# Performance work log

Measured on AMD Instinct MI355X. Metric: run time of the kernel, lower is better.

## Reference

```python
import jax, jax.numpy as jnp
import numpy as np

IN_CH = 1024
OUT_CH = 1024
N_SUBJECTS = 32
B = 512


def setup_inputs() -> dict:
    key = jax.random.key(0)
    k_x, k_w, k_b, k_idx = jax.random.split(key, 4)
    scale = 1.0 / (IN_CH ** 0.5)
    x = jax.random.normal(k_x, (B, IN_CH), dtype=jnp.float32)
    weights = jax.random.normal(k_w, (N_SUBJECTS, IN_CH, OUT_CH), dtype=jnp.float32) * scale
    bias = jax.random.normal(k_b, (N_SUBJECTS, OUT_CH), dtype=jnp.float32) * scale
    subject_idx = jax.random.randint(k_idx, (B,), 0, N_SUBJECTS, dtype=jnp.int64)
    return {"x": x, "subject_idx": subject_idx, "weights": weights, "bias": bias}


def reference(x, subject_idx, weights, bias):
    # gather per-sample weight [B,C,D] and bias [B,D]
    w = weights[subject_idx]          # [B, C, D]
    b = bias[subject_idx]             # [B, D]
    out = jnp.einsum('bc,bcd->bd', x, w) + b
    return out
```

## Files before the change

kernel.cpp:

```cpp
#include <hip/hip_runtime.h>
#include <hip/hip_bf16.h>


typedef float f4v __attribute__((ext_vector_type(4)));

#define N_SUBJ 32
#define B_ROWS 512
#define IN_CH_K 1024
#define OUT_CH_K 1024
#define RPC 24
#define MAX_CHUNKS 64
#define CSEGS 4
#define CSEG 256
#define WSLICE 64
#define DTILES 4
#define DTILE 256
#define XPAD 28

#define ENT_OFF 1
#define PERM_OFF 256

__global__ __launch_bounds__(512) void build_groups(
    const int* __restrict__ idx, int* __restrict__ ws)
{
    __shared__ int counts[N_SUBJ];
    __shared__ int offs[N_SUBJ];
    __shared__ int cursor[N_SUBJ];
    const int t = threadIdx.x;
    if (t < N_SUBJ) counts[t] = 0;
    __syncthreads();
    const int s = idx[t] & (N_SUBJ - 1);
    atomicAdd(&counts[s], 1);
    __syncthreads();
    if (t == 0) {
        int acc = 0, nch = 0;
        for (int i = 0; i < N_SUBJ; ++i) {
            offs[i] = acc;
            cursor[i] = acc;
            acc += counts[i];
        }
        for (int i = 0; i < N_SUBJ; ++i) {
            for (int st = 0; st < counts[i]; st += RPC) {
                int c = counts[i] - st;
                if (c > RPC) c = RPC;
                ws[ENT_OFF + nch * 3 + 0] = i;
                ws[ENT_OFF + nch * 3 + 1] = offs[i] + st;
                ws[ENT_OFF + nch * 3 + 2] = c;
                ++nch;
            }
        }
        ws[0] = nch;
    }
    __syncthreads();
    const int pos = atomicAdd(&cursor[s], 1);
    ws[PERM_OFF + pos] = t;
}

__global__ __launch_bounds__(256) void init_bias(
    const int* __restrict__ idx, const float* __restrict__ bias,
    float* __restrict__ out)
{
    const int b = blockIdx.x;
    const int s = idx[b];
    const int d = threadIdx.x * 4;
    *(float4*)&out[(size_t)b * OUT_CH_K + d] =
        *(const float4*)&bias[(size_t)s * OUT_CH_K + d];
}

#define GLOAD(dst, ptr) \
    asm volatile("global_load_dwordx4 %0, %1, off" : "=v"(dst) : "v"(ptr))
#define WAIT_VM(n) do { \
    asm volatile("s_waitcnt vmcnt(" #n ")" ::: "memory"); \
    __builtin_amdgcn_sched_barrier(0); } while (0)

#define CSTEP(wreg, cidx) { \
    const float4 x0 = ((const float4*)&xst[cidx][0])[0]; \
    const float4 x1 = ((const float4*)&xst[cidx][0])[1]; \
    const float4 x2 = ((const float4*)&xst[cidx][0])[2]; \
    const float4 x3 = ((const float4*)&xst[cidx][0])[3]; \
    const float4 x4 = ((const float4*)&xst[cidx][0])[4]; \
    const float4 x5 = ((const float4*)&xst[cidx][0])[5]; \
    acc[ 0] += wreg * x0.x;  acc[ 1] += wreg * x0.y; \
    acc[ 2] += wreg * x0.z;  acc[ 3] += wreg * x0.w; \
    acc[ 4] += wreg * x1.x;  acc[ 5] += wreg * x1.y; \
    acc[ 6] += wreg * x1.z;  acc[ 7] += wreg * x1.w; \
    acc[ 8] += wreg * x2.x;  acc[ 9] += wreg * x2.y; \
    acc[10] += wreg * x2.z;  acc[11] += wreg * x2.w; \
    acc[12] += wreg * x3.x;  acc[13] += wreg * x3.y; \
    acc[14] += wreg * x3.z;  acc[15] += wreg * x3.w; \
    acc[16] += wreg * x4.x;  acc[17] += wreg * x4.y; \
    acc[18] += wreg * x4.z;  acc[19] += wreg * x4.w; \
    acc[20] += wreg * x5.x;  acc[21] += wreg * x5.y; \
    acc[22] += wreg * x5.z;  acc[23] += wreg * x5.w; }

__global__ __launch_bounds__(256, 2) void subject_gemm(
    const float* __restrict__ x, const float* __restrict__ W,
    const int* __restrict__ ws, float* __restrict__ out)
{
    const int chunk = blockIdx.x;
    if (chunk >= ws[0]) return;
    const int s     = ws[ENT_OFF + chunk * 3 + 0];
    const int start = ws[ENT_OFF + chunk * 3 + 1];
    const int cnt   = ws[ENT_OFF + chunk * 3 + 2];
    const int cbase = blockIdx.y * CSEG;
    const int dbase = blockIdx.z * DTILE;

    __shared__ float xst[CSEG][XPAD];
    __shared__ int rowidx[RPC];

    const int t = threadIdx.x;
    if (t < RPC)
        rowidx[t] = (t < cnt) ? ws[PERM_OFF + start + t] : -1;
    __syncthreads();

    #pragma unroll
    for (int r = 0; r < RPC; ++r) {
        const int row = rowidx[r];
        xst[t][r] = (row >= 0) ? x[(size_t)row * IN_CH_K + cbase + t] : 0.0f;
    }
    __syncthreads();

    const int lane = t & 63;
    const int wave = t >> 6;
    const int cs   = wave * WSLICE;
    const int d    = dbase + lane * 4;
    const float* wp = W + (size_t)s * (IN_CH_K * OUT_CH_K)
                        + (size_t)(cbase + cs) * OUT_CH_K + d;

    f4v acc[RPC];
    #pragma unroll
    for (int r = 0; r < RPC; ++r) acc[r] = (f4v){0.f, 0.f, 0.f, 0.f};
    f4v wa0, wa1, wa2, wa3, wb0, wb1, wb2, wb3;

    GLOAD(wa0, wp + 0 * OUT_CH_K);
    GLOAD(wa1, wp + 1 * OUT_CH_K);
    GLOAD(wa2, wp + 2 * OUT_CH_K);
    GLOAD(wa3, wp + 3 * OUT_CH_K);
    GLOAD(wb0, wp + 4 * OUT_CH_K);
    GLOAD(wb1, wp + 5 * OUT_CH_K);
    GLOAD(wb2, wp + 6 * OUT_CH_K);
    GLOAD(wb3, wp + 7 * OUT_CH_K);

    #pragma unroll 1
    for (int cb = 0; cb < WSLICE - 8; cb += 8) {
        WAIT_VM(4);
        CSTEP(wa0, cs + cb + 0)
        CSTEP(wa1, cs + cb + 1)
        CSTEP(wa2, cs + cb + 2)
        CSTEP(wa3, cs + cb + 3)
        const float* wn = wp + (size_t)(cb + 8) * OUT_CH_K;
        GLOAD(wa0, wn + 0 * OUT_CH_K);
        GLOAD(wa1, wn + 1 * OUT_CH_K);
        GLOAD(wa2, wn + 2 * OUT_CH_K);
        GLOAD(wa3, wn + 3 * OUT_CH_K);
        WAIT_VM(4);
        CSTEP(wb0, cs + cb + 4)
        CSTEP(wb1, cs + cb + 5)
        CSTEP(wb2, cs + cb + 6)
        CSTEP(wb3, cs + cb + 7)
        GLOAD(wb0, wn + 4 * OUT_CH_K);
        GLOAD(wb1, wn + 5 * OUT_CH_K);
        GLOAD(wb2, wn + 6 * OUT_CH_K);
        GLOAD(wb3, wn + 7 * OUT_CH_K);
    }
    {
        const int cb = WSLICE - 8;
        WAIT_VM(4);
        CSTEP(wa0, cs + cb + 0)
        CSTEP(wa1, cs + cb + 1)
        CSTEP(wa2, cs + cb + 2)
        CSTEP(wa3, cs + cb + 3)
        WAIT_VM(0);
        CSTEP(wb0, cs + cb + 4)
        CSTEP(wb1, cs + cb + 5)
        CSTEP(wb2, cs + cb + 6)
        CSTEP(wb3, cs + cb + 7)
    }

    __syncthreads();
    float (*obuf)[DTILE] = (float(*)[DTILE])&xst[0][0];
    if (wave == 0) {
        #pragma unroll
        for (int r = 0; r < RPC; ++r)
            *(f4v*)&obuf[r][lane * 4] = acc[r];
    }
    __syncthreads();
    #pragma unroll
    for (int w = 1; w < 4; ++w) {
        if (wave == w) {
            #pragma unroll
            for (int r = 0; r < RPC; ++r) {
                f4v v = *(const f4v*)&obuf[r][lane * 4];
                *(f4v*)&obuf[r][lane * 4] = v + acc[r];
            }
        }
        __syncthreads();
    }

    #pragma unroll
    for (int i = 0; i < 6; ++i) {
        const int r = wave * 6 + i;
        const int row = rowidx[r];
        if (row >= 0) {
            const f4v v = *(const f4v*)&obuf[r][lane * 4];
            float* o = &out[(size_t)row * OUT_CH_K + d];
            atomicAdd(o + 0, v.x); atomicAdd(o + 1, v.y);
            atomicAdd(o + 2, v.z); atomicAdd(o + 3, v.w);
        }
    }
}

extern "C" void kernel_launch(void* const* d_in, const int* in_sizes, int n_in,
                              void* d_out, int out_size, void* d_ws, size_t ws_size,
                              hipStream_t stream) {
    const float* x    = (const float*)d_in[0];
    const int*   idx  = (const int*)d_in[1];
    const float* W    = (const float*)d_in[2];
    const float* bias = (const float*)d_in[3];
    float* out = (float*)d_out;
    int* ws = (int*)d_ws;

    build_groups<<<1, 512, 0, stream>>>(idx, ws);
    init_bias<<<B_ROWS, 256, 0, stream>>>(idx, bias, out);

    dim3 grid(MAX_CHUNKS, CSEGS, DTILES);
    subject_gemm<<<grid, 256, 0, stream>>>(x, W, ws, out);
}
```

Before: 234.6 us.

## Split reduction into eight C segments with partial buffers and separate reduce kernel

Doubles the number of input-channel segments (CSEG 256→128), which doubles the GEMM grid so more blocks are available to cover the weight stream. Atomic float adds into the output are replaced by plain vector stores into per-segment partial buffers in workspace. A new reduce kernel sums the eight partials and adds the bias, and it replaces the old bias-init kernel. The cost is extra workspace traffic of 8×512×1024 floats written and read, plus the assumption that every (row, segment) partial slot is written, which holds because each row belongs to exactly one chunk.

New measurement: 233.3 us. Within noise of the previous version (-0.5%).

```diff
diff --git a/kernel.cpp b/kernel.cpp
--- a/kernel.cpp
+++ b/kernel.cpp
@@ -10,15 +10,16 @@
 #define OUT_CH_K 1024
 #define RPC 24
 #define MAX_CHUNKS 64
-#define CSEGS 4
-#define CSEG 256
-#define WSLICE 64
+#define CSEGS 8
+#define CSEG 128
+#define WSLICE 32
 #define DTILES 4
 #define DTILE 256
 #define XPAD 28
 
 #define ENT_OFF 1
 #define PERM_OFF 256
+#define PART_OFF_F 1024
 
 __global__ __launch_bounds__(512) void build_groups(
     const int* __restrict__ idx, int* __restrict__ ws)
@@ -54,17 +55,6 @@
     __syncthreads();
     const int pos = atomicAdd(&cursor[s], 1);
     ws[PERM_OFF + pos] = t;
-}
-
-__global__ __launch_bounds__(256) void init_bias(
-    const int* __restrict__ idx, const float* __restrict__ bias,
-    float* __restrict__ out)
-{
-    const int b = blockIdx.x;
-    const int s = idx[b];
-    const int d = threadIdx.x * 4;
-    *(float4*)&out[(size_t)b * OUT_CH_K + d] =
-        *(const float4*)&bias[(size_t)s * OUT_CH_K + d];
 }
 
 #define GLOAD(dst, ptr) \
@@ -95,7 +85,7 @@
 
 __global__ __launch_bounds__(256, 2) void subject_gemm(
     const float* __restrict__ x, const float* __restrict__ W,
-    const int* __restrict__ ws, float* __restrict__ out)
+    const int* __restrict__ ws, float* __restrict__ ws_part)
 {
     const int chunk = blockIdx.x;
     if (chunk >= ws[0]) return;
@@ -105,7 +95,8 @@
     const int cbase = blockIdx.y * CSEG;
     const int dbase = blockIdx.z * DTILE;
 
-    __shared__ float xst[CSEG][XPAD];
+    __shared__ float smem[RPC * DTILE];
+    float (*xst)[XPAD] = (float(*)[XPAD])smem;
     __shared__ int rowidx[RPC];
 
     const int t = threadIdx.x;
@@ -113,10 +104,13 @@
         rowidx[t] = (t < cnt) ? ws[PERM_OFF + start + t] : -1;
     __syncthreads();
 
-    #pragma unroll
-    for (int r = 0; r < RPC; ++r) {
-        const int row = rowidx[r];
-        xst[t][r] = (row >= 0) ? x[(size_t)row * IN_CH_K + cbase + t] : 0.0f;
+    const int tc  = t & 127;
+    const int tr2 = t >> 7;
+    #pragma unroll
+    for (int r = 0; r < RPC; r += 2) {
+        const int rr  = r + tr2;
+        const int row = rowidx[rr];
+        xst[tc][rr] = (row >= 0) ? x[(size_t)row * IN_CH_K + cbase + tc] : 0.0f;
     }
     __syncthreads();
 
@@ -178,7 +172,7 @@
     }
 
     __syncthreads();
-    float (*obuf)[DTILE] = (float(*)[DTILE])&xst[0][0];
+    float (*obuf)[DTILE] = (float(*)[DTILE])smem;
     if (wave == 0) {
         #pragma unroll
         for (int r = 0; r < RPC; ++r)
@@ -197,17 +191,32 @@
         __syncthreads();
     }
 
+    float* pb = ws_part + (size_t)blockIdx.y * (B_ROWS * OUT_CH_K) + d;
     #pragma unroll
     for (int i = 0; i < 6; ++i) {
         const int r = wave * 6 + i;
         const int row = rowidx[r];
-        if (row >= 0) {
-            const f4v v = *(const f4v*)&obuf[r][lane * 4];
-            float* o = &out[(size_t)row * OUT_CH_K + d];
-            atomicAdd(o + 0, v.x); atomicAdd(o + 1, v.y);
-            atomicAdd(o + 2, v.z); atomicAdd(o + 3, v.w);
-        }
-    }
+        if (row >= 0)
+            *(f4v*)(pb + (size_t)row * OUT_CH_K) =
+                *(const f4v*)&obuf[r][lane * 4];
+    }
+}
+
+__global__ __launch_bounds__(256) void reduce_parts(
+    const int* __restrict__ idx, const float* __restrict__ bias,
+    const float* __restrict__ part, float* __restrict__ out)
+{
+    const int b = blockIdx.x;
+    const int s = idx[b];
+    const int d = threadIdx.x * 4;
+    float4 a = *(const float4*)&bias[(size_t)s * OUT_CH_K + d];
+    #pragma unroll
+    for (int k = 0; k < CSEGS; ++k) {
+        const float4 p = *(const float4*)
+            &part[((size_t)k * B_ROWS + b) * OUT_CH_K + d];
+        a.x += p.x; a.y += p.y; a.z += p.z; a.w += p.w;
+    }
+    *(float4*)&out[(size_t)b * OUT_CH_K + d] = a;
 }
 
 extern "C" void kernel_launch(void* const* d_in, const int* in_sizes, int n_in,
@@ -219,10 +228,11 @@
     const float* bias = (const float*)d_in[3];
     float* out = (float*)d_out;
     int* ws = (int*)d_ws;
+    float* ws_part = (float*)ws + PART_OFF_F;
 
     build_groups<<<1, 512, 0, stream>>>(idx, ws);
-    init_bias<<<B_ROWS, 256, 0, stream>>>(idx, bias, out);
 
     dim3 grid(MAX_CHUNKS, CSEGS, DTILES);
-    subject_gemm<<<grid, 256, 0, stream>>>(x, W, ws, out);
-}
+    subject_gemm<<<grid, 256, 0, stream>>>(x, W, ws, ws_part);
+    reduce_parts<<<B_ROWS, 256, 0, stream>>>(idx, bias, ws_part, out);
+}
```
